# Kernel optimization log

Measured on AMD Instinct MI355X. Metric: run time of the kernel, lower is better.

Reference implementation:

```python
import jax, jax.numpy as jnp
import numpy as np

B, P, D = 8, 196, 768       # batch, patches per image, hidden
H, DH = 12, 64              # heads, head dim (H*DH == D)
L = 4                       # GAT layers
THRESH = 0.1                # GraphGenerator similarity threshold
SLOPE = 0.2                 # LeakyReLU negative slope (DGL GATConv default)
NEG = -1e9


def setup_inputs() -> dict:
    key = jax.random.key(0)
    k0, k1, k2, k3, k4 = jax.random.split(key, 5)
    l_feat = jax.random.normal(k0, (B, P, D), jnp.float32)
    r_feat = jax.random.normal(k1, (B, P, D), jnp.float32)
    W = jax.random.normal(k2, (L, D, H * DH), jnp.float32) / np.float32(np.sqrt(D))
    a_src = jax.random.normal(k3, (L, H, DH), jnp.float32) / np.float32(np.sqrt(DH))
    a_dst = jax.random.normal(k4, (L, H, DH), jnp.float32) / np.float32(np.sqrt(DH))
    b = jnp.zeros((L, H * DH), jnp.float32)
    return dict(l_feat=l_feat, r_feat=r_feat, W=W, a_src=a_src, a_dst=a_dst, b=b)


def _leaky(x):
    return jax.nn.leaky_relu(x, SLOPE)


def _gat_layer_bipartite(h, Wl, a_s, a_d, bias, mask_rl, Nl):
    # Graph: edges l->r where mask_rl[r, l] is True, plus a self loop on every node.
    # l-nodes therefore only see themselves (alpha = 1).
    N = h.shape[0]
    z = (h @ Wl).reshape(N, H, DH)                      # [N, H, DH]
    el = jnp.einsum('nhd,hd->nh', z, a_s)               # src score
    er = jnp.einsum('nhd,hd->nh', z, a_d)               # dst score
    zl, zr = z[:Nl], z[Nl:]
    cross = _leaky(el[:Nl][None, :, :] + er[Nl:][:, None, :])   # [Nr, Nl, H]
    cross = jnp.where(mask_rl[..., None], cross, NEG)
    self_r = _leaky(el[Nl:] + er[Nl:])                   # [Nr, H] self-loop logit
    logits = jnp.concatenate([cross, self_r[:, None, :]], axis=1)  # [Nr, Nl+1, H]
    alpha = jax.nn.softmax(logits, axis=1)
    out_r = jnp.einsum('rlh,lhd->rhd', alpha[:, :Nl], zl) + alpha[:, Nl][..., None] * zr
    out = jnp.concatenate([zl, out_r], axis=0)           # l-nodes: identity (self loop)
    return out.reshape(N, H * DH) + bias


def _gat_layer_pool(h, Wl, a_s, a_d, bias):
    # Graph from _gather: every node -> first node of its P-block (col = img_node
    # repeat_interleave) plus add_self_loop. The root's self edge thus appears TWICE,
    # giving it multiplicity 2 in the edge softmax. Non-root nodes: self loop only.
    N = h.shape[0]
    G = N // P
    z = (h @ Wl).reshape(G, P, H, DH)
    el = jnp.einsum('gphd,hd->gph', z, a_s)
    er = jnp.einsum('gphd,hd->gph', z, a_d)
    logits = _leaky(el + er[:, :1, :])                   # [G, P, H], dst = node 0
    logc = jnp.log(jnp.where(jnp.arange(P) == 0, 2.0, 1.0)).astype(h.dtype)
    alpha = jax.nn.softmax(logits + logc[None, :, None], axis=1)
    pooled = jnp.einsum('gph,gphd->ghd', alpha, z)       # root aggregation
    out = z.at[:, 0].set(pooled)                         # others keep self value
    return out.reshape(N, H * DH) + bias


def _gat(h, W, a_src, a_dst, b, layer_fn):
    for i in range(L):
        h = layer_fn(h, W[i], a_src[i], a_dst[i], b[i])
        if i < L - 1:
            h = jax.nn.elu(h)
    return h


def reference(l_feat, r_feat, W, a_src, a_dst, b):
    node_l = l_feat.reshape(-1, D)
    node_r = r_feat.reshape(-1, D)
    Nl = node_l.shape[0]
    # GraphGenerator: cosine-similarity threshold graph (edges l -> r)
    nl = node_l / jnp.linalg.norm(node_l, axis=-1, keepdims=True)
    nr = node_r / jnp.linalg.norm(node_r, axis=-1, keepdims=True)
    mask_rl = (nr @ nl.T) > THRESH                       # [Nr, Nl]
    h = jnp.concatenate([node_l, node_r], axis=0)        # [2*B*P, D]
    h = _gat(h, W, a_src, a_dst, b,
             lambda x, w, s, d, bb: _gat_layer_bipartite(x, w, s, d, bb, mask_rl, Nl))
    # second GAT pass on the pooling graph, then index_select the per-image roots
    h = _gat(h, W, a_src, a_dst, b, _gat_layer_pool)
    img = h[::P]                                         # img_node = arange(0, N, P)
    return img[:B], img[B:]                              # (node_feat_l, node_feat_r)
```

## Files before the change

### kernel.cpp

```cpp
#include <hip/hip_runtime.h>
#include <math.h>

#define NL    1568
#define NTOT  3136
#define DD    768
#define NH    12
#define DHD   64
#define WPR   49
#define MAXDEG 64
#define NKSTEP 24
#define LOG2F_ 0.69314718055994530942f

typedef _Float16 h8 __attribute__((ext_vector_type(8)));
typedef float f32x4 __attribute__((ext_vector_type(4)));
#define MFMA16(a, b, c) __builtin_amdgcn_mfma_f32_16x16x32_f16(a, b, c, 0, 0, 0)

__device__ __forceinline__ float leaky(float x) { return x > 0.f ? x : 0.2f * x; }

__device__ __forceinline__ void gld16(const _Float16* g, _Float16* l) {
  __builtin_amdgcn_global_load_lds(
      (const __attribute__((address_space(1))) void*)g,
      (__attribute__((address_space(3))) void*)l, 16, 0, 0);
}

__global__ __launch_bounds__(192) void conv_init(const float* __restrict__ lf, const float* __restrict__ rf,
                                                 _Float16* __restrict__ hi, float* __restrict__ norms) {
  int n = blockIdx.x;
  int t = threadIdx.x;
  const float* src = (n < NL) ? lf + (size_t)n * DD : rf + (size_t)(n - NL) * DD;
  float4 v = reinterpret_cast<const float4*>(src)[t];
  typedef _Float16 h4v __attribute__((ext_vector_type(4)));
  h4v hv = {(_Float16)v.x, (_Float16)v.y, (_Float16)v.z, (_Float16)v.w};
  reinterpret_cast<h4v*>(hi)[(size_t)n * (DD / 4) + t] = hv;
  float s = v.x * v.x + v.y * v.y + v.z * v.z + v.w * v.w;
  #pragma unroll
  for (int o = 32; o; o >>= 1) s += __shfl_xor(s, o);
  __shared__ float red[3];
  if ((t & 63) == 0) red[t >> 6] = s;
  __syncthreads();
  if (t == 0) norms[n] = sqrtf(red[0] + red[1] + red[2]);
}

__global__ __launch_bounds__(256) void transp_W(const float* __restrict__ W, _Float16* __restrict__ Wthi) {
  __shared__ float tile[32][33];
  int kt = blockIdx.x * 32, nt = blockIdx.y * 32, i = blockIdx.z;
  int tx = threadIdx.x & 31, ty = threadIdx.x >> 5;
  const float* Wp = W + ((size_t)i * DD + kt) * DD + nt;
  #pragma unroll
  for (int p = 0; p < 4; ++p) tile[ty + p * 8][tx] = Wp[(size_t)(ty + p * 8) * DD + tx];
  __syncthreads();
  _Float16* oh = Wthi + ((size_t)i * DD + nt) * DD + kt;
  #pragma unroll
  for (int p = 0; p < 4; ++p) {
    int nn = ty + p * 8;
    oh[(size_t)nn * DD + tx] = (_Float16)tile[tx][nn];
  }
}

__global__ __launch_bounds__(256) void gemm_mfma(const _Float16* __restrict__ Ahi,
                                                 const _Float16* __restrict__ Bhi,
                                                 const float* __restrict__ a_s, const float* __restrict__ a_d,
                                                 const float* __restrict__ bias,
                                                 _Float16* __restrict__ zh,
                                                 float* __restrict__ el, float* __restrict__ er,
                                                 _Float16* __restrict__ ohhi,
                                                 int do_elu, int mode) {
  __shared__ _Float16 sm[2][2][2048];
  int t = threadIdx.x;
  int xcd = blockIdx.x & 7, pos = blockIdx.x >> 3;
  int orig = (xcd < 4 ? xcd * 74 : 296 + (xcd - 4) * 73) + pos;
  int bx = orig / 12, by = orig % 12;
  int m0 = bx * 64, n0 = by * 64;

  int rl = t >> 2;
  int kq_src = (t & 3) ^ ((t >> 3) & 3);
  size_t aoff = (size_t)(m0 + rl) * DD + kq_src * 8;
  size_t boff = (size_t)(n0 + rl) * DD + kq_src * 8;
  const _Float16* pAhi = Ahi + aoff;
  const _Float16* pBhi = Bhi + boff;
  int ch = (t >> 6) * 512;

  int ln = t & 63, wv = t >> 6;
  int fr = ln & 15, kg = ln >> 4;
  int kq8 = (kg ^ ((fr >> 1) & 3)) * 8;
  int aRead = (wv * 16 + fr) * 32 + kq8;

  f32x4 zero = {0.f, 0.f, 0.f, 0.f};
  f32x4 acc[4];
  #pragma unroll
  for (int cg = 0; cg < 4; ++cg) acc[cg] = zero;

  gld16(pAhi, &sm[0][0][ch]);
  gld16(pBhi, &sm[0][1][ch]);
  __syncthreads();

  for (int step = 0; step < NKSTEP; ++step) {
    int buf = step & 1;
    if (step < NKSTEP - 1) {
      int kb = (step + 1) * 32;
      gld16(pAhi + kb, &sm[buf ^ 1][0][ch]);
      gld16(pBhi + kb, &sm[buf ^ 1][1][ch]);
    }
    h8 ah = *reinterpret_cast<const h8*>(&sm[buf][0][aRead]);
    #pragma unroll
    for (int cg = 0; cg < 4; ++cg) {
      int bRead = (cg * 16 + fr) * 32 + kq8;
      h8 bh = *reinterpret_cast<const h8*>(&sm[buf][1][bRead]);
      acc[cg] = MFMA16(ah, bh, acc[cg]);
    }
    __syncthreads();
  }

  int head = by;
  int orow = m0 + wv * 16 + kg * 4;
  #pragma unroll
  for (int i = 0; i < 4; ++i) {
    int r = orow + i;
    bool wh = (mode == 0) ? (r < NL) : (r % 196 != 0);
    #pragma unroll
    for (int cg = 0; cg < 4; ++cg) {
      int c = n0 + cg * 16 + fr;
      float z = acc[cg][i];
      zh[(size_t)r * DD + c] = (_Float16)z;
      if (wh) {
        float o = z + bias[c];
        if (do_elu) o = o > 0.f ? o : expm1f(o);
        ohhi[(size_t)r * DD + c] = (_Float16)o;
      }
    }
  }
  float asv[4], adv[4];
  #pragma unroll
  for (int cg = 0; cg < 4; ++cg) {
    asv[cg] = a_s[head * DHD + cg * 16 + fr];
    adv[cg] = a_d[head * DHD + cg * 16 + fr];
  }
  #pragma unroll
  for (int i = 0; i < 4; ++i) {
    float s1 = 0.f, s2 = 0.f;
    #pragma unroll
    for (int cg = 0; cg < 4; ++cg) {
      s1 = fmaf(acc[cg][i], asv[cg], s1);
      s2 = fmaf(acc[cg][i], adv[cg], s2);
    }
    #pragma unroll
    for (int o = 1; o < 16; o <<= 1) {
      s1 += __shfl_xor(s1, o);
      s2 += __shfl_xor(s2, o);
    }
    if (fr == 0) {
      el[(size_t)(orow + i) * NH + head] = s1;
      er[(size_t)(orow + i) * NH + head] = s2;
    }
  }
}

__global__ __launch_bounds__(256) void mask_mfma(const _Float16* __restrict__ Hhi,
                                                 const float* __restrict__ lf, const float* __restrict__ rf,
                                                 const float* __restrict__ norms, unsigned* __restrict__ mask) {
  __shared__ _Float16 sm[2][2][2048];
  __shared__ unsigned mw[64][2];
  int t = threadIdx.x;
  int r0 = blockIdx.x * 64, l0 = blockIdx.y * 64;

  int rl = t >> 2;
  int kq_src = (t & 3) ^ ((t >> 3) & 3);
  int ra = r0 + rl; if (ra >= NL) ra = NL - 1;
  int la = l0 + rl; if (la >= NL) la = NL - 1;
  const _Float16* pA = Hhi + (size_t)(NL + ra) * DD + kq_src * 8;
  const _Float16* pB = Hhi + (size_t)la * DD + kq_src * 8;
  int ch = (t >> 6) * 512;

  int ln = t & 63, wv = t >> 6;
  int fr = ln & 15, kg = ln >> 4;
  int kq8 = (kg ^ ((fr >> 1) & 3)) * 8;
  int aRead = (wv * 16 + fr) * 32 + kq8;

  f32x4 zero = {0.f, 0.f, 0.f, 0.f};
  f32x4 acc[4];
  #pragma unroll
  for (int cg = 0; cg < 4; ++cg) acc[cg] = zero;
  if (t < 128) mw[t >> 1][t & 1] = 0u;

  gld16(pA, &sm[0][0][ch]);
  gld16(pB, &sm[0][1][ch]);
  __syncthreads();

  for (int step = 0; step < NKSTEP; ++step) {
    int buf = step & 1;
    if (step < NKSTEP - 1) {
      int kb = (step + 1) * 32;
      gld16(pA + kb, &sm[buf ^ 1][0][ch]);
      gld16(pB + kb, &sm[buf ^ 1][1][ch]);
    }
    h8 ah = *reinterpret_cast<const h8*>(&sm[buf][0][aRead]);
    #pragma unroll
    for (int cg = 0; cg < 4; ++cg) {
      int bRead = (cg * 16 + fr) * 32 + kq8;
      h8 bh = *reinterpret_cast<const h8*>(&sm[buf][1][bRead]);
      acc[cg] = MFMA16(ah, bh, acc[cg]);
    }
    __syncthreads();
  }

  int rloc = wv * 16 + kg * 4;
  float nrv[4];
  #pragma unroll
  for (int i = 0; i < 4; ++i) {
    int r = r0 + rloc + i;
    nrv[i] = norms[NL + (r < NL ? r : NL - 1)];
  }
  #pragma unroll
  for (int cg = 0; cg < 4; ++cg) {
    int lloc = cg * 16 + fr;
    int l = l0 + lloc;
    float nlv = norms[l < NL ? l : NL - 1];
    #pragma unroll
    for (int i = 0; i < 4; ++i) {
      int r = r0 + rloc + i;
      if (r >= NL || l >= NL) continue;
      float thr = 0.1f * nrv[i] * nlv;
      float dot = acc[cg][i];
      bool bit;
      if (fabsf(dot - thr) <= 0.5f) {
        const float4* rp = reinterpret_cast<const float4*>(rf + (size_t)r * DD);
        const float4* lp = reinterpret_cast<const float4*>(lf + (size_t)l * DD);
        float s = 0.f;
        #pragma unroll 4
        for (int k = 0; k < DD / 4; ++k) {
          float4 a = rp[k], b = lp[k];
          s = fmaf(a.x, b.x, s); s = fmaf(a.y, b.y, s);
          s = fmaf(a.z, b.z, s); s = fmaf(a.w, b.w, s);
        }
        bit = s > thr;
      } else {
        bit = dot > thr;
      }
      if (bit) atomicOr(&mw[rloc + i][lloc >> 5], 1u << (lloc & 31));
    }
  }
  __syncthreads();
  if (t < 128) {
    int rr = t >> 1, w = t & 1;
    int rg = r0 + rr, wg = blockIdx.y * 2 + w;
    if (rg < NL && wg < WPR) mask[(size_t)rg * WPR + wg] = mw[rr][w];
  }
}

__global__ __launch_bounds__(64) void build_csr(const unsigned* __restrict__ mask,
                                                int* __restrict__ nbr, int* __restrict__ deg) {
  int r = blockIdx.x * 64 + threadIdx.x;
  if (r >= NL) return;
  const unsigned* mr = mask + (size_t)r * WPR;
  int* out = nbr + (size_t)r * MAXDEG;
  int cnt = 0;
  #pragma unroll 7
  for (int w = 0; w < WPR; ++w) {
    unsigned m = mr[w];
    while (m) {
      int bpos = __ffs(m) - 1;
      m &= m - 1;
      if (cnt < MAXDEG) out[cnt] = w * 32 + bpos;
      ++cnt;
    }
  }
  deg[r] = cnt < MAXDEG ? cnt : MAXDEG;
}

__global__ __launch_bounds__(768) void bip_fused(const _Float16* __restrict__ zh, const float* __restrict__ el,
                                                 const float* __restrict__ er, const int* __restrict__ nbr,
                                                 const int* __restrict__ deg, const float* __restrict__ bias,
                                                 _Float16* __restrict__ ohhi,
                                                 int do_elu) {
  int r = blockIdx.x;
  int R = NL + r;
  int t = threadIdx.x;
  int dg = deg[r];
  __shared__ int nb_s[MAXDEG];
  __shared__ float wbuf[MAXDEG * NH];
  __shared__ float den_s[NH], wself_s[NH];
  if (t < dg) nb_s[t] = nbr[(size_t)r * MAXDEG + t];
  __syncthreads();
  if (t < dg * NH) {
    int j = t / NH, h2 = t - j * NH;
    wbuf[t] = el[(size_t)nb_s[j] * NH + h2];
  }
  __syncthreads();
  if (t < NH) {
    float er_r = er[(size_t)R * NH + t];
    float s = leaky(el[(size_t)R * NH + t] + er_r);
    float mx = s;
    for (int j = 0; j < dg; ++j) mx = fmaxf(mx, leaky(wbuf[j * NH + t] + er_r));
    float den = 0.f;
    for (int j = 0; j < dg; ++j) {
      float w = expf(leaky(wbuf[j * NH + t] + er_r) - mx);
      wbuf[j * NH + t] = w;
      den += w;
    }
    float ws = expf(s - mx);
    den_s[t] = den + ws;
    wself_s[t] = ws;
  }
  __syncthreads();
  int h2 = t >> 6;
  float acc = wself_s[h2] * (float)zh[(size_t)R * DD + t];
  for (int j = 0; j < dg; ++j)
    acc = fmaf(wbuf[j * NH + h2], (float)zh[(size_t)nb_s[j] * DD + t], acc);
  float o = acc / den_s[h2] + bias[t];
  if (do_elu) o = o > 0.f ? o : expm1f(o);
  ohhi[(size_t)R * DD + t] = (_Float16)o;
}

__global__ __launch_bounds__(256) void pool_attn2(const _Float16* __restrict__ zh, const float* __restrict__ el,
                                                  const float* __restrict__ er, const float* __restrict__ bias,
                                                  _Float16* __restrict__ ohhi,
                                                  float* __restrict__ root_out, int do_elu) {
  int g = blockIdx.x, h = blockIdx.y;
  int base = g * 196;
  int t = threadIdx.x;
  int w = t >> 6, d = t & 63;
  __shared__ float wb[196];
  __shared__ float red[4];
  __shared__ float accP[4][64];
  float er0 = er[(size_t)base * NH + h];
  float lg = -INFINITY;
  if (t < 196) {
    lg = leaky(el[(size_t)(base + t) * NH + h] + er0);
    if (t == 0) lg += LOG2F_;
  }
  float m = lg;
  #pragma unroll
  for (int o = 32; o; o >>= 1) m = fmaxf(m, __shfl_xor(m, o));
  if ((t & 63) == 0) red[w] = m;
  __syncthreads();
  float mx = fmaxf(fmaxf(red[0], red[1]), fmaxf(red[2], red[3]));
  float wgt = (t < 196) ? expf(lg - mx) : 0.f;
  if (t < 196) wb[t] = wgt;
  float dn = wgt;
  #pragma unroll
  for (int o = 32; o; o >>= 1) dn += __shfl_xor(dn, o);
  __syncthreads();
  if ((t & 63) == 0) red[w] = dn;
  __syncthreads();
  float den = red[0] + red[1] + red[2] + red[3];
  float acc = 0.f;
  int p0 = w * 49;
  #pragma unroll 7
  for (int p = p0; p < p0 + 49; ++p)
    acc = fmaf(wb[p], (float)zh[(size_t)(base + p) * DD + h * DHD + d], acc);
  accP[w][d] = acc;
  __syncthreads();
  if (w == 0) {
    float o = (accP[0][d] + accP[1][d] + accP[2][d] + accP[3][d]) / den + bias[h * DHD + d];
    if (do_elu) o = o > 0.f ? o : expm1f(o);
    int c = h * DHD + d;
    ohhi[(size_t)base * DD + c] = (_Float16)o;
    root_out[(size_t)g * DD + c] = o;
  }
}

extern "C" void kernel_launch(void* const* d_in, const int* in_sizes, int n_in,
                              void* d_out, int out_size, void* d_ws, size_t ws_size,
                              hipStream_t stream) {
  const float* l_feat = (const float*)d_in[0];
  const float* r_feat = (const float*)d_in[1];
  const float* W      = (const float*)d_in[2];
  const float* a_src  = (const float*)d_in[3];
  const float* a_dst  = (const float*)d_in[4];
  const float* b      = (const float*)d_in[5];
  float* out = (float*)d_out;

  float* el    = (float*)d_ws;
  float* er    = el + (size_t)NTOT * NH;
  float* norms = er + (size_t)NTOT * NH;
  float* hroot = norms + NTOT;
  unsigned* mask = (unsigned*)(hroot + 16 * DD);
  int* nbr = (int*)(mask + (size_t)NL * WPR);
  int* deg = nbr + (size_t)NL * MAXDEG;
  _Float16* hhiA = (_Float16*)(deg + NL);
  _Float16* hhiB = hhiA + (size_t)NTOT * DD;
  _Float16* Wthi = hhiB + (size_t)NTOT * DD;
  _Float16* zh   = Wthi + (size_t)4 * DD * DD;

  _Float16* hhi[2] = {hhiA, hhiB};

  conv_init<<<NTOT, 192, 0, stream>>>(l_feat, r_feat, hhiA, norms);
  transp_W<<<dim3(24, 24, 4), 256, 0, stream>>>(W, Wthi);
  mask_mfma<<<dim3(25, 25), 256, 0, stream>>>(hhiA, l_feat, r_feat, norms, mask);
  build_csr<<<(NL + 63) / 64, 64, 0, stream>>>(mask, nbr, deg);

  for (int i = 0; i < 4; ++i) {
    const float* bi = b + (size_t)i * DD;
    int do_elu = (i < 3) ? 1 : 0;
    int ib = i & 1, ob = (i + 1) & 1;
    gemm_mfma<<<588, 256, 0, stream>>>(hhi[ib],
        Wthi + (size_t)i * DD * DD,
        a_src + (size_t)i * NH * DHD, a_dst + (size_t)i * NH * DHD,
        bi, zh, el, er, hhi[ob], do_elu, 0);
    bip_fused<<<NL, 768, 0, stream>>>(zh, el, er, nbr, deg, bi, hhi[ob], do_elu);
  }

  for (int i = 0; i < 4; ++i) {
    const float* bi = b + (size_t)i * DD;
    int do_elu = (i < 3) ? 1 : 0;
    int L = 4 + i;
    int ib = L & 1, ob = (L + 1) & 1;
    gemm_mfma<<<588, 256, 0, stream>>>(hhi[ib],
        Wthi + (size_t)i * DD * DD,
        a_src + (size_t)i * NH * DHD, a_dst + (size_t)i * NH * DHD,
        bi, zh, el, er, hhi[ob], do_elu, 1);
    pool_attn2<<<dim3(16, NH), 256, 0, stream>>>(zh, el, er, bi, hhi[ob],
        (i == 3) ? out : hroot, do_elu);
  }
}
```

Measured before the change: 289.1 us.

## Defer borderline mask recomputation to a separate wave-parallel fix-up kernel

The fp16 MFMA mask kernel no longer recomputes near-threshold dot products in fp32 serially per thread. It appends the borderline (r,l) pairs to a global list through an atomic counter, and a new mask_fix kernel recomputes each pair with one wavefront and a shuffle reduction, then sets or clears the bit atomically. This removes divergent, uncoalesced 768-length serial loops from the MFMA kernel. It adds a memset, an extra launch and a fixed list capacity; pairs beyond LISTCAP would silently keep their fp16 decision.

```diff
diff --git a/kernel.cpp b/kernel.cpp
--- a/kernel.cpp
+++ b/kernel.cpp
@@ -9,6 +9,7 @@
 #define WPR   49
 #define MAXDEG 64
 #define NKSTEP 24
+#define LISTCAP 16384
 #define LOG2F_ 0.69314718055994530942f
 
 typedef _Float16 h8 __attribute__((ext_vector_type(8)));
@@ -156,8 +157,8 @@
 }
 
 __global__ __launch_bounds__(256) void mask_mfma(const _Float16* __restrict__ Hhi,
-                                                 const float* __restrict__ lf, const float* __restrict__ rf,
-                                                 const float* __restrict__ norms, unsigned* __restrict__ mask) {
+                                                 const float* __restrict__ norms, unsigned* __restrict__ mask,
+                                                 unsigned* __restrict__ bcnt, int2* __restrict__ blist) {
   __shared__ _Float16 sm[2][2][2048];
   __shared__ unsigned mw[64][2];
   int t = threadIdx.x;
@@ -221,22 +222,11 @@
       if (r >= NL || l >= NL) continue;
       float thr = 0.1f * nrv[i] * nlv;
       float dot = acc[cg][i];
-      bool bit;
       if (fabsf(dot - thr) <= 0.5f) {
-        const float4* rp = reinterpret_cast<const float4*>(rf + (size_t)r * DD);
-        const float4* lp = reinterpret_cast<const float4*>(lf + (size_t)l * DD);
-        float s = 0.f;
-        #pragma unroll 4
-        for (int k = 0; k < DD / 4; ++k) {
-          float4 a = rp[k], b = lp[k];
-          s = fmaf(a.x, b.x, s); s = fmaf(a.y, b.y, s);
-          s = fmaf(a.z, b.z, s); s = fmaf(a.w, b.w, s);
-        }
-        bit = s > thr;
-      } else {
-        bit = dot > thr;
+        unsigned pos = atomicAdd(bcnt, 1u);
+        if (pos < LISTCAP) blist[pos] = make_int2(r, l);
       }
-      if (bit) atomicOr(&mw[rloc + i][lloc >> 5], 1u << (lloc & 31));
+      if (dot > thr) atomicOr(&mw[rloc + i][lloc >> 5], 1u << (lloc & 31));
     }
   }
   __syncthreads();
@@ -244,6 +234,38 @@
     int rr = t >> 1, w = t & 1;
     int rg = r0 + rr, wg = blockIdx.y * 2 + w;
     if (rg < NL && wg < WPR) mask[(size_t)rg * WPR + wg] = mw[rr][w];
+  }
+}
+
+__global__ __launch_bounds__(256) void mask_fix(const float* __restrict__ lf, const float* __restrict__ rf,
+                                                const float* __restrict__ norms,
+                                                const unsigned* __restrict__ bcnt, const int2* __restrict__ blist,
+                                                unsigned* __restrict__ mask) {
+  unsigned cnt = *bcnt;
+  if (cnt > LISTCAP) cnt = LISTCAP;
+  int lane = threadIdx.x & 63;
+  unsigned wid = blockIdx.x * 4 + (threadIdx.x >> 6);
+  for (unsigned idx = wid; idx < cnt; idx += gridDim.x * 4) {
+    int2 pr = blist[idx];
+    int r = pr.x, l = pr.y;
+    const float4* rp = reinterpret_cast<const float4*>(rf + (size_t)r * DD);
+    const float4* lp = reinterpret_cast<const float4*>(lf + (size_t)l * DD);
+    float s = 0.f;
+    #pragma unroll
+    for (int k = 0; k < 3; ++k) {
+      float4 a = rp[lane + k * 64], b = lp[lane + k * 64];
+      s = fmaf(a.x, b.x, s); s = fmaf(a.y, b.y, s);
+      s = fmaf(a.z, b.z, s); s = fmaf(a.w, b.w, s);
+    }
+    #pragma unroll
+    for (int o = 32; o; o >>= 1) s += __shfl_xor(s, o);
+    if (lane == 0) {
+      float thr = 0.1f * norms[NL + r] * norms[l];
+      unsigned* wp = &mask[(size_t)r * WPR + (l >> 5)];
+      unsigned bit = 1u << (l & 31);
+      if (s > thr) atomicOr(wp, bit);
+      else atomicAnd(wp, ~bit);
+    }
   }
 }
 
@@ -381,12 +403,16 @@
   _Float16* hhiB = hhiA + (size_t)NTOT * DD;
   _Float16* Wthi = hhiB + (size_t)NTOT * DD;
   _Float16* zh   = Wthi + (size_t)4 * DD * DD;
+  unsigned* bcnt = (unsigned*)(zh + (size_t)NTOT * DD);
+  int2* blist    = (int2*)(bcnt + 2);
 
   _Float16* hhi[2] = {hhiA, hhiB};
 
   conv_init<<<NTOT, 192, 0, stream>>>(l_feat, r_feat, hhiA, norms);
   transp_W<<<dim3(24, 24, 4), 256, 0, stream>>>(W, Wthi);
-  mask_mfma<<<dim3(25, 25), 256, 0, stream>>>(hhiA, l_feat, r_feat, norms, mask);
+  hipMemsetAsync(bcnt, 0, 4, stream);
+  mask_mfma<<<dim3(25, 25), 256, 0, stream>>>(hhiA, norms, mask, bcnt, blist);
+  mask_fix<<<32, 256, 0, stream>>>(l_feat, r_feat, norms, bcnt, blist, mask);
   build_csr<<<(NL + 63) / 64, 64, 0, stream>>>(mask, nbr, deg);
 
   for (int i = 0; i < 4; ++i) {
```

Result: faster. 268.6 us (-7.1%).
